# Kernel optimization log

Hardware: AMD Instinct MI355X
Metric: run time of the kernel (lower is better)

The kernel has to match this reference:

```python
import jax, jax.numpy as jnp
import numpy as np

N = 2048
D_T = 256; D_F = 256
E_T = 32; E_F = 32; E_C = 128
C = 5; Q = 512


def setup_inputs() -> dict:
    key = jax.random.key(0)
    ks = jax.random.split(key, 12)
    # full graph minus self-loops, row-major (matches dense_to_sparse ordering)
    r, c = np.meshgrid(np.arange(N), np.arange(N), indexing='ij')
    m = r != c
    edge_index = jnp.asarray(np.stack([r[m], c[m]]), dtype=jnp.int32)  # [2, N*(N-1)]
    E = edge_index.shape[1]
    s = 0.02
    return {
        'time_features': jax.random.normal(ks[0], (N, D_T), jnp.float32),
        'edge_index': edge_index,
        'time_edge_weight': jax.random.uniform(ks[1], (E,), jnp.float32),
        'freq_features': jax.random.normal(ks[2], (N, D_F), jnp.float32),
        'freq_edge_weight': jax.random.uniform(ks[3], (E,), jnp.float32),
        'labels': jax.random.randint(ks[4], (N,), 0, C, jnp.int32),
        'num_classes': C,
        'query_size': Q,
        'Wt': jax.random.normal(ks[5], (D_T, E_T), jnp.float32) * s,
        'bt': jnp.zeros((E_T,), jnp.float32),
        'Wf': jax.random.normal(ks[6], (D_F, E_F), jnp.float32) * s,
        'bf': jnp.zeros((E_F,), jnp.float32),
        'Wc': jax.random.normal(ks[7], (E_T + E_F + C, E_C), jnp.float32) * s,
        'bc': jnp.zeros((E_C,), jnp.float32),
        'Wo': jax.random.normal(ks[8], (E_C, C), jnp.float32) * s,
        'bo': jnp.zeros((C,), jnp.float32),
    }


def _gcn(x, A, W, b):
    # torch_geometric GCNConv: D^{-1/2}(A + I)D^{-1/2} (X W) + b
    n = A.shape[0]
    Ah = A + jnp.eye(n, dtype=A.dtype)
    deg = Ah.sum(axis=1)
    dis = jnp.where(deg > 0, jax.lax.rsqrt(deg), 0.0)
    return (dis[:, None] * Ah * dis[None, :]) @ (x @ W) + b


def reference(time_features, edge_index, time_edge_weight, freq_features,
              freq_edge_weight, labels, num_classes, query_size,
              Wt, bt, Wf, bf, Wc, bc, Wo, bo):
    n = time_features.shape[0]
    lrelu = lambda z: jax.nn.leaky_relu(z, 0.01)

    def dense_adj(w):  # A[dst, src] = w
        return jnp.zeros((n, n), w.dtype).at[edge_index[1], edge_index[0]].add(w)

    te = lrelu(_gcn(time_features, dense_adj(time_edge_weight), Wt, bt))
    fe = lrelu(_gcn(freq_features, dense_adj(freq_edge_weight), Wf, bf))

    # to_one_hot: one_hot[:n - query_size, labels] = 1 -> support rows get 1 in
    # every column that appears anywhere in `labels`
    cols = jnp.zeros((num_classes,), te.dtype).at[labels].set(1.0)
    rowmask = (jnp.arange(n) < (n - query_size)).astype(te.dtype)
    one_hot = rowmask[:, None] * cols[None, :]

    feats = jnp.concatenate([te, fe, one_hot], axis=-1)  # [n, E_T+E_F+C]

    # graph_construction (no_grad in original): 1 / (L1 distance over the
    # non-one-hot dims + 1e-5), zero diagonal
    fd = jax.lax.stop_gradient(feats[:, : feats.shape[1] - num_classes])
    dist = jnp.sum(jnp.abs(fd[:, None, :] - fd[None, :, :]), axis=-1)  # [n, n]
    Aw = (1.0 / (dist + 1e-5)) * (1.0 - jnp.eye(n, dtype=feats.dtype))

    emb = lrelu(_gcn(feats, Aw, Wc, bc))
    return emb @ Wo + bo
```

## Files before the change

### kernel.cpp

```cpp
#include <hip/hip_runtime.h>
#include <hip/hip_bf16.h>

#define N 2048
#define NM1 2047
#define DT 256
#define ET 32
#define EC 128
#define NC 5
#define FS 80
#define FD 69
#define KC_ET 16
#define KC_EC 16

typedef __hip_bfloat16 bf16;

__global__ __launch_bounds__(256) void k_deg_label_xw(const float* __restrict__ tw,
                                                      const float* __restrict__ fw,
                                                      const int* __restrict__ labels,
                                                      const float* __restrict__ Xt,
                                                      const float* __restrict__ Wt,
                                                      const float* __restrict__ Xf,
                                                      const float* __restrict__ Wf,
                                                      float* __restrict__ degT,
                                                      float* __restrict__ degF,
                                                      float* __restrict__ cols,
                                                      float* __restrict__ Yt,
                                                      float* __restrict__ Yf){
    int b = blockIdx.x;
    int t = threadIdx.x;
    if (b < 512){
        int p = (b & 7)*256 + t;
        if (p >= NM1) return;
        int s0 = (b >> 3)*32;
        float lowT=0.f, highT=0.f, lowF=0.f, highF=0.f;
        #pragma unroll 8
        for (int r = 0; r < 32; ++r){
            int s = s0 + r;
            float vt = tw[(size_t)s*NM1 + p];
            float vf = fw[(size_t)s*NM1 + p];
            if (s <= p){ highT += vt; highF += vf; }
            else       { lowT  += vt; lowF  += vf; }
        }
        atomicAdd(&degT[p],   lowT);
        atomicAdd(&degF[p],   lowF);
        atomicAdd(&degT[p+1], highT);
        atomicAdd(&degF[p+1], highF);
        return;
    }
    if (b == 512){
        __shared__ float lc[NC];
        if (t < NC) lc[t] = 0.f;
        __syncthreads();
        for (int i = t; i < N; i += 256){
            int l = labels[i];
            if (l >= 0 && l < NC) lc[l] = 1.f;
        }
        __syncthreads();
        if (t < NC) cols[t] = lc[t];
        return;
    }
    int idx = b - 513;
    const float* X = (idx & 256) ? Xf : Xt;
    const float* W = (idx & 256) ? Wf : Wt;
    float*       Y = (idx & 256) ? Yf : Yt;
    __shared__ float Ws[DT*ET];
    __shared__ float Xs[8*DT];
    for (int j = t; j < DT*ET; j += 256) Ws[j] = W[j];
    int i0 = (idx & 255)*8;
    for (int j = t; j < 8*DT; j += 256) Xs[j] = X[(size_t)i0*DT + j];
    __syncthreads();
    int r = t >> 5, f = t & 31;
    const float* xr = Xs + r*DT;
    float acc = 0.f;
    #pragma unroll 8
    for (int d = 0; d < DT; ++d) acc += xr[d]*Ws[d*ET+f];
    Y[(size_t)(i0+r)*ET+f] = acc;
}

__global__ __launch_bounds__(256) void k_agg_et(const float* __restrict__ tw,
                                                const float* __restrict__ fw,
                                                const float* __restrict__ Yt,
                                                const float* __restrict__ Yf,
                                                const float* __restrict__ degT,
                                                const float* __restrict__ degF,
                                                float* __restrict__ Pt,
                                                float* __restrict__ Pf){
    __shared__ float Ast[64*68];
    __shared__ float Asf[64*68];
    __shared__ float Zst[64*ET];
    __shared__ float Zsf[64*ET];
    int t = threadIdx.x;
    int i0 = blockIdx.x*64;
    int kc = blockIdx.y;
    int k0 = kc*128;
    int g  = t >> 7;
    int tt = t & 127;
    int ig = tt >> 3, fg = tt & 7;
    int r0 = ig*4, c0 = fg*4;
    const float* As = g ? Asf : Ast;
    const float* Zs = g ? Zsf : Zst;
    float acc[4][4];
    #pragma unroll
    for (int u=0;u<4;++u)
        #pragma unroll
        for (int v=0;v<4;++v) acc[u][v]=0.f;

    for (int kt = 0; kt < 2; ++kt){
        int kb = k0 + kt*64;
        #pragma unroll
        for (int e = 0; e < 16; ++e){
            int id = t + e*256;
            int k_l = id >> 6, i_l = id & 63;
            int k = kb + k_l;
            int gi = i0 + i_l;
            float vt, vf;
            if (gi == k){ vt = 0.f; vf = 0.f; }
            else {
                size_t base = (size_t)k*NM1 + gi - (gi > k ? 1 : 0);
                vt = tw[base]; vf = fw[base];
            }
            Ast[k_l*68 + i_l] = vt;
            Asf[k_l*68 + i_l] = vf;
        }
        #pragma unroll
        for (int e = 0; e < 2; ++e){
            int id = t + e*256;
            int row = id >> 3;
            int c4  = (id & 7)*4;
            float rdT = rsqrtf(1.f + degT[kb+row]);
            float rdF = rsqrtf(1.f + degF[kb+row]);
            float4 yt = *(const float4*)&Yt[(size_t)(kb+row)*ET + c4];
            float4 yf = *(const float4*)&Yf[(size_t)(kb+row)*ET + c4];
            yt.x*=rdT; yt.y*=rdT; yt.z*=rdT; yt.w*=rdT;
            yf.x*=rdF; yf.y*=rdF; yf.z*=rdF; yf.w*=rdF;
            *(float4*)&Zst[row*ET + c4] = yt;
            *(float4*)&Zsf[row*ET + c4] = yf;
        }
        __syncthreads();
        for (int k = 0; k < 64; ++k){
            float4 a = *(const float4*)&As[k*68 + r0];
            float4 z = *(const float4*)&Zs[k*ET + c0];
            const float* ap = (const float*)&a;
            const float* zp = (const float*)&z;
            #pragma unroll
            for (int u = 0; u < 4; ++u)
                #pragma unroll
                for (int v = 0; v < 4; ++v)
                    acc[u][v] += ap[u]*zp[v];
        }
        __syncthreads();
    }
    float* P = g ? Pf : Pt;
    #pragma unroll
    for (int u = 0; u < 4; ++u){
        size_t ii = (size_t)(i0 + r0 + u);
        float4 o;
        float* po = (float*)&o;
        #pragma unroll
        for (int v = 0; v < 4; ++v) po[v]=acc[u][v];
        *(float4*)&P[(size_t)kc*(N*ET) + ii*ET + c0] = o;
    }
}

__global__ __launch_bounds__(256) void k_feats_epi(const float* __restrict__ Pt,
                                                   const float* __restrict__ Pf,
                                                   const float* __restrict__ Yt,
                                                   const float* __restrict__ Yf,
                                                   const float* __restrict__ degT,
                                                   const float* __restrict__ degF,
                                                   const float* __restrict__ bt,
                                                   const float* __restrict__ bfv,
                                                   const float* __restrict__ cols,
                                                   const int* __restrict__ qsize,
                                                   float* __restrict__ feats){
    int idx = blockIdx.x*256 + threadIdx.x;
    int i = idx >> 6;
    int f = idx & 63;
    float s, rd, b;
    if (f < ET){
        rd = rsqrtf(1.f + degT[i]);
        s = rd*Yt[(size_t)i*ET + f];
        #pragma unroll
        for (int kc = 0; kc < KC_ET; ++kc) s += Pt[(size_t)kc*(N*ET) + (size_t)i*ET + f];
        b = bt[f];
    } else {
        int g = f - ET;
        rd = rsqrtf(1.f + degF[i]);
        s = rd*Yf[(size_t)i*ET + g];
        #pragma unroll
        for (int kc = 0; kc < KC_ET; ++kc) s += Pf[(size_t)kc*(N*ET) + (size_t)i*ET + g];
        b = bfv[g];
    }
    float v = rd*s + b;
    feats[(size_t)i*FS + f] = v > 0.f ? v : 0.01f*v;
    if (f < NC){
        int nsup = N - qsize[0];
        feats[(size_t)i*FS + 2*ET + f] = (i < nsup) ? cols[f] : 0.f;
    }
}

__global__ __launch_bounds__(256) void k_build_aw(const float* __restrict__ feats,
                                                  float* __restrict__ Aw,
                                                  float* __restrict__ dsum){
    __shared__ float fiT[64*68];
    __shared__ float fjT[64*68];
    int t = threadIdx.x;
    int i0 = blockIdx.x*64, j0 = blockIdx.y*64;
    {
        int row = t >> 2;
        int cb  = (t & 3)*16;
        const float4* si = (const float4*)(feats + (size_t)(i0+row)*FS + cb);
        const float4* sj = (const float4*)(feats + (size_t)(j0+row)*FS + cb);
        #pragma unroll
        for (int s = 0; s < 4; ++s){
            float4 v = si[s];
            float4 w = sj[s];
            int c = cb + s*4;
            fiT[(c+0)*68+row]=v.x; fiT[(c+1)*68+row]=v.y; fiT[(c+2)*68+row]=v.z; fiT[(c+3)*68+row]=v.w;
            fjT[(c+0)*68+row]=w.x; fjT[(c+1)*68+row]=w.y; fjT[(c+2)*68+row]=w.z; fjT[(c+3)*68+row]=w.w;
        }
    }
    __syncthreads();
    int tx = t & 15, ty = t >> 4;
    float acc[4][4];
    #pragma unroll
    for (int u=0;u<4;++u)
        #pragma unroll
        for (int v=0;v<4;++v) acc[u][v]=0.f;
    for (int d = 0; d < 64; ++d){
        float4 a4 = *(const float4*)&fiT[d*68 + ty*4];
        float4 b4 = *(const float4*)&fjT[d*68 + tx*4];
        const float* ap = (const float*)&a4;
        const float* bp = (const float*)&b4;
        #pragma unroll
        for (int u = 0; u < 4; ++u)
            #pragma unroll
            for (int v = 0; v < 4; ++v)
                acc[u][v] += fabsf(ap[u]-bp[v]);
    }
    #pragma unroll
    for (int u = 0; u < 4; ++u){
        int gi = i0 + ty*4 + u;
        float4 o;
        float* po = (float*)&o;
        #pragma unroll
        for (int v = 0; v < 4; ++v){
            int gj = j0 + tx*4 + v;
            po[v] = (gi==gj) ? 1.0f : 1.0f/(acc[u][v] + 1e-5f);
        }
        *(float4*)&Aw[(size_t)gi*N + j0 + tx*4] = o;
        float rs = (po[0]+po[1]) + (po[2]+po[3]);
        rs += __shfl_xor(rs, 1);
        rs += __shfl_xor(rs, 2);
        rs += __shfl_xor(rs, 4);
        rs += __shfl_xor(rs, 8);
        if (tx == 0) atomicAdd(&dsum[gi], rs);
    }
}

__global__ __launch_bounds__(256) void k_featswc(const float* __restrict__ feats,
                                                 const float* __restrict__ Wc,
                                                 const float* __restrict__ dsum,
                                                 float* __restrict__ Zc){
    __shared__ float Wcs[FD*EC];
    __shared__ float fr[8][FD+3];
    int t = threadIdx.x;
    for (int idx = t; idx < FD*EC; idx += 256) Wcs[idx] = Wc[idx];
    int i0 = blockIdx.x*8;
    for (int idx = t; idx < 8*FD; idx += 256){
        int r = idx / FD;
        int c = idx - r*FD;
        fr[r][c] = feats[(size_t)(i0+r)*FS + c];
    }
    __syncthreads();
    int f  = t & 127;
    int rh = t >> 7;
    for (int rr = 0; rr < 4; ++rr){
        int r = rh*4 + rr;
        float acc = 0.f;
        #pragma unroll
        for (int d = 0; d < FD; ++d) acc += fr[r][d]*Wcs[d*EC+f];
        int i = i0 + r;
        Zc[(size_t)i*EC + f] = rsqrtf(dsum[i])*acc;
    }
}

__global__ __launch_bounds__(256) void k_agg_ec(const float* __restrict__ Aw,
                                                const float* __restrict__ Zc,
                                                float* __restrict__ Pe){
    __shared__ float As[128*128];
    __shared__ float Zs[128*128];
    int t = threadIdx.x;
    int i0 = blockIdx.x*128;
    int kc = blockIdx.y;
    int k0 = kc*128;
    int rg = t >> 4;
    int cg = t & 15;
    int r0 = rg*8;
    int ca = cg*4, cb = 64 + cg*4;

    #pragma unroll
    for (int e = 0; e < 16; ++e){
        int id = t + e*256;
        int k_l = id >> 5;
        int i4  = (id & 31)*4;
        *(float4*)&As[k_l*128 + i4] = *(const float4*)&Aw[(size_t)(k0+k_l)*N + i0 + i4];
    }
    #pragma unroll
    for (int e = 0; e < 16; ++e){
        int id = t + e*256;
        int k_l = id >> 5;
        int c4  = (id & 31)*4;
        *(float4*)&Zs[k_l*128 + c4] = *(const float4*)&Zc[(size_t)(k0+k_l)*EC + c4];
    }
    __syncthreads();

    float acc[8][8];
    #pragma unroll
    for (int u=0;u<8;++u)
        #pragma unroll
        for (int v=0;v<8;++v) acc[u][v]=0.f;

    for (int k = 0; k < 128; ++k){
        float4 a0 = *(const float4*)&As[k*128 + r0];
        float4 a1 = *(const float4*)&As[k*128 + r0 + 4];
        float4 z0 = *(const float4*)&Zs[k*128 + ca];
        float4 z1 = *(const float4*)&Zs[k*128 + cb];
        float a8[8] = {a0.x,a0.y,a0.z,a0.w,a1.x,a1.y,a1.z,a1.w};
        float zl[4] = {z0.x,z0.y,z0.z,z0.w};
        float zh[4] = {z1.x,z1.y,z1.z,z1.w};
        #pragma unroll
        for (int u = 0; u < 8; ++u){
            #pragma unroll
            for (int v = 0; v < 4; ++v){
                acc[u][v]   += a8[u]*zl[v];
                acc[u][v+4] += a8[u]*zh[v];
            }
        }
    }
    #pragma unroll
    for (int u = 0; u < 8; ++u){
        size_t ii = (size_t)(i0 + r0 + u);
        float4 o0, o1;
        float* p0 = (float*)&o0; float* p1 = (float*)&o1;
        #pragma unroll
        for (int v = 0; v < 4; ++v){ p0[v]=acc[u][v]; p1[v]=acc[u][v+4]; }
        *(float4*)&Pe[(size_t)kc*(N*EC) + ii*EC + ca] = o0;
        *(float4*)&Pe[(size_t)kc*(N*EC) + ii*EC + cb] = o1;
    }
}

__global__ __launch_bounds__(256) void k_embfinal(const float* __restrict__ Pe,
                                                  const float* __restrict__ dsum,
                                                  const float* __restrict__ bc,
                                                  const float* __restrict__ Wo,
                                                  const float* __restrict__ bo,
                                                  float* __restrict__ out){
    __shared__ float vs[2][EC];
    __shared__ float Wos[EC*NC];
    __shared__ float bos[NC];
    int t = threadIdx.x;
    for (int idx = t; idx < EC*NC; idx += 256) Wos[idx] = Wo[idx];
    if (t < NC) bos[t] = bo[t];
    int rr = t >> 7, f = t & 127;
    int i = blockIdx.x*2 + rr;
    size_t idx = (size_t)i*EC + f;
    float s = 0.f;
    #pragma unroll
    for (int kc = 0; kc < KC_EC; ++kc) s += Pe[(size_t)kc*(N*EC) + idx];
    float v = rsqrtf(dsum[i])*s + bc[f];
    vs[rr][f] = v > 0.f ? v : 0.01f*v;
    __syncthreads();
    if (t < 2*NC){
        int r = t / NC;
        int c = t - r*NC;
        float a = bos[c];
        #pragma unroll 8
        for (int f2 = 0; f2 < EC; ++f2) a += vs[r][f2]*Wos[f2*NC+c];
        out[(size_t)(blockIdx.x*2 + r)*NC + c] = a;
    }
}

extern "C" void kernel_launch(void* const* d_in, const int* in_sizes, int n_in,
                              void* d_out, int out_size, void* d_ws, size_t ws_size,
                              hipStream_t stream) {
    const float* time_features = (const float*)d_in[0];
    const float* tw            = (const float*)d_in[2];
    const float* freq_features = (const float*)d_in[3];
    const float* fw            = (const float*)d_in[4];
    const int*   labels        = (const int*)d_in[5];
    const int*   qsize         = (const int*)d_in[7];
    const float* Wt  = (const float*)d_in[8];
    const float* bt  = (const float*)d_in[9];
    const float* Wf  = (const float*)d_in[10];
    const float* bfv = (const float*)d_in[11];
    const float* Wc  = (const float*)d_in[12];
    const float* bc  = (const float*)d_in[13];
    const float* Wo  = (const float*)d_in[14];
    const float* bo  = (const float*)d_in[15];
    float* out = (float*)d_out;

    float* ws    = (float*)d_ws;
    float* Yt    = ws;
    float* Yf    = Yt + (size_t)N*ET;
    float* Zc    = Yf + (size_t)N*ET;
    float* degT  = Zc + (size_t)N*EC;
    float* degF  = degT + N;
    float* dsum  = degF + N;
    float* colsb = dsum + N;
    float* feats = colsb + 8;
    float* Aw    = feats + (size_t)N*FS;
    float* Pt    = Aw + (size_t)N*N;
    float* Pf    = Pt + (size_t)KC_ET*N*ET;
    float* Pe    = Pf + (size_t)KC_ET*N*ET;

    hipMemsetAsync(degT, 0, 3*N*sizeof(float), stream);
    k_deg_label_xw<<<1025, 256, 0, stream>>>(tw, fw, labels,
                                             time_features, Wt, freq_features, Wf,
                                             degT, degF, colsb, Yt, Yf);
    k_agg_et<<<dim3(N/64, KC_ET), 256, 0, stream>>>(tw, fw, Yt, Yf, degT, degF, Pt, Pf);
    k_feats_epi<<<(N*64)/256, 256, 0, stream>>>(Pt, Pf, Yt, Yf, degT, degF,
                                                bt, bfv, colsb, qsize, feats);
    k_build_aw<<<dim3(N/64, N/64), 256, 0, stream>>>(feats, Aw, dsum);
    k_featswc<<<N/8, 256, 0, stream>>>(feats, Wc, dsum, Zc);
    k_agg_ec<<<dim3(N/128, KC_EC), 256, 0, stream>>>(Aw, Zc, Pe);
    k_embfinal<<<N/2, 256, 0, stream>>>(Pe, dsum, bc, Wo, bo, out);
}
```

Measured before the change: 209.1 us.

## Fuse all stages into one persistent kernel with software grid barriers

```diff
diff --git a/kernel.cpp b/kernel.cpp
--- a/kernel.cpp
+++ b/kernel.cpp
@@ -11,373 +11,372 @@
 #define FD 69
 #define KC_ET 16
 #define KC_EC 16
+#define NB 256
 
 typedef __hip_bfloat16 bf16;
 
-__global__ __launch_bounds__(256) void k_deg_label_xw(const float* __restrict__ tw,
-                                                      const float* __restrict__ fw,
-                                                      const int* __restrict__ labels,
-                                                      const float* __restrict__ Xt,
-                                                      const float* __restrict__ Wt,
-                                                      const float* __restrict__ Xf,
-                                                      const float* __restrict__ Wf,
-                                                      float* __restrict__ degT,
-                                                      float* __restrict__ degF,
-                                                      float* __restrict__ cols,
-                                                      float* __restrict__ Yt,
-                                                      float* __restrict__ Yf){
+__device__ __forceinline__ void gridbar(int* cnt, int target){
+    __syncthreads();
+    if (threadIdx.x == 0){
+        __threadfence();
+        atomicAdd(cnt, 1);
+        while (atomicAdd(cnt, 0) < target) __builtin_amdgcn_s_sleep(1);
+        __threadfence();
+    }
+    __syncthreads();
+}
+
+__global__ __launch_bounds__(256, 1)
+void k_mega(const float* __restrict__ tw, const float* __restrict__ fw,
+            const int* __restrict__ labels,
+            const float* __restrict__ Xt, const float* __restrict__ Wt,
+            const float* __restrict__ Xf, const float* __restrict__ Wf,
+            const float* __restrict__ bt, const float* __restrict__ bfv,
+            const int* __restrict__ qsize,
+            const float* __restrict__ Wc, const float* __restrict__ bc,
+            const float* __restrict__ Wo, const float* __restrict__ bo,
+            float* degT, float* degF, float* dsum, int* cnt, float* colsb,
+            float* Yt, float* Yf, float* Zc, float* feats, float* Aw,
+            float* Pt, float* Pf, float* Pe, float* out){
+    __shared__ float lds[32768];
     int b = blockIdx.x;
     int t = threadIdx.x;
-    if (b < 512){
-        int p = (b & 7)*256 + t;
-        if (p >= NM1) return;
-        int s0 = (b >> 3)*32;
-        float lowT=0.f, highT=0.f, lowF=0.f, highF=0.f;
-        #pragma unroll 8
-        for (int r = 0; r < 32; ++r){
-            int s = s0 + r;
-            float vt = tw[(size_t)s*NM1 + p];
-            float vf = fw[(size_t)s*NM1 + p];
-            if (s <= p){ highT += vt; highF += vf; }
-            else       { lowT  += vt; lowF  += vf; }
-        }
-        atomicAdd(&degT[p],   lowT);
-        atomicAdd(&degF[p],   lowF);
-        atomicAdd(&degT[p+1], highT);
-        atomicAdd(&degF[p+1], highF);
-        return;
-    }
-    if (b == 512){
-        __shared__ float lc[NC];
-        if (t < NC) lc[t] = 0.f;
+
+    for (int v = b; v < 1025; v += NB){
+        if (v < 512){
+            int p = (v & 7)*256 + t;
+            if (p < NM1){
+                int s0 = (v >> 3)*32;
+                float lowT=0.f, highT=0.f, lowF=0.f, highF=0.f;
+                #pragma unroll 8
+                for (int r = 0; r < 32; ++r){
+                    int s = s0 + r;
+                    float vt = tw[(size_t)s*NM1 + p];
+                    float vf = fw[(size_t)s*NM1 + p];
+                    if (s <= p){ highT += vt; highF += vf; }
+                    else       { lowT  += vt; lowF  += vf; }
+                }
+                atomicAdd(&degT[p],   lowT);
+                atomicAdd(&degF[p],   lowF);
+                atomicAdd(&degT[p+1], highT);
+                atomicAdd(&degF[p+1], highF);
+            }
+        } else if (v == 512){
+            float* lc = lds;
+            if (t < NC) lc[t] = 0.f;
+            __syncthreads();
+            for (int i = t; i < N; i += 256){
+                int l = labels[i];
+                if (l >= 0 && l < NC) lc[l] = 1.f;
+            }
+            __syncthreads();
+            if (t < NC) colsb[t] = lc[t];
+            __syncthreads();
+        } else {
+            int idx = v - 513;
+            const float* X = (idx & 256) ? Xf : Xt;
+            const float* W = (idx & 256) ? Wf : Wt;
+            float*       Y = (idx & 256) ? Yf : Yt;
+            float* Ws = lds;
+            float* Xs = lds + 8192;
+            for (int j = t; j < DT*ET; j += 256) Ws[j] = W[j];
+            int i0 = (idx & 255)*8;
+            for (int j = t; j < 8*DT; j += 256) Xs[j] = X[(size_t)i0*DT + j];
+            __syncthreads();
+            int r = t >> 5, f = t & 31;
+            const float* xr = Xs + r*DT;
+            float acc = 0.f;
+            #pragma unroll 8
+            for (int d = 0; d < DT; ++d) acc += xr[d]*Ws[d*ET+f];
+            Y[(size_t)(i0+r)*ET+f] = acc;
+            __syncthreads();
+        }
+    }
+    gridbar(cnt, 1*NB);
+
+    {
+        float* Ast = lds;
+        float* Asf = lds + 64*68;
+        float* Zst = lds + 2*64*68;
+        float* Zsf = lds + 2*64*68 + 64*32;
+        int g  = t >> 7;
+        int tt = t & 127;
+        int ig = tt >> 3, fg = tt & 7;
+        int r0 = ig*4, c0 = fg*4;
+        const float* As = g ? Asf : Ast;
+        const float* Zs = g ? Zsf : Zst;
+        for (int vv = 0; vv < 2; ++vv){
+            int v = b*2 + vv;
+            int i0 = (v & 31)*64;
+            int kc = v >> 5;
+            int k0 = kc*128;
+            float acc[4][4];
+            #pragma unroll
+            for (int u=0;u<4;++u)
+                #pragma unroll
+                for (int w=0;w<4;++w) acc[u][w]=0.f;
+            for (int kt = 0; kt < 2; ++kt){
+                int kb = k0 + kt*64;
+                #pragma unroll
+                for (int e = 0; e < 16; ++e){
+                    int id = t + e*256;
+                    int k_l = id >> 6, i_l = id & 63;
+                    int k = kb + k_l;
+                    int gi = i0 + i_l;
+                    float vt, vf;
+                    if (gi == k){ vt = 0.f; vf = 0.f; }
+                    else {
+                        size_t base = (size_t)k*NM1 + gi - (gi > k ? 1 : 0);
+                        vt = tw[base]; vf = fw[base];
+                    }
+                    Ast[k_l*68 + i_l] = vt;
+                    Asf[k_l*68 + i_l] = vf;
+                }
+                #pragma unroll
+                for (int e = 0; e < 2; ++e){
+                    int id = t + e*256;
+                    int row = id >> 3;
+                    int c4  = (id & 7)*4;
+                    float rdT = rsqrtf(1.f + degT[kb+row]);
+                    float rdF = rsqrtf(1.f + degF[kb+row]);
+                    float4 yt = *(const float4*)&Yt[(size_t)(kb+row)*ET + c4];
+                    float4 yf = *(const float4*)&Yf[(size_t)(kb+row)*ET + c4];
+                    yt.x*=rdT; yt.y*=rdT; yt.z*=rdT; yt.w*=rdT;
+                    yf.x*=rdF; yf.y*=rdF; yf.z*=rdF; yf.w*=rdF;
+                    *(float4*)&Zst[row*ET + c4] = yt;
+                    *(float4*)&Zsf[row*ET + c4] = yf;
+                }
+                __syncthreads();
+                for (int k = 0; k < 64; ++k){
+                    float4 a = *(const float4*)&As[k*68 + r0];
+                    float4 z = *(const float4*)&Zs[k*ET + c0];
+                    const float* ap = (const float*)&a;
+                    const float* zp = (const float*)&z;
+                    #pragma unroll
+                    for (int u = 0; u < 4; ++u)
+                        #pragma unroll
+                        for (int w = 0; w < 4; ++w)
+                            acc[u][w] += ap[u]*zp[w];
+                }
+                __syncthreads();
+            }
+            float* P = g ? Pf : Pt;
+            #pragma unroll
+            for (int u = 0; u < 4; ++u){
+                size_t ii = (size_t)(i0 + r0 + u);
+                float4 o;
+                float* po = (float*)&o;
+                #pragma unroll
+                for (int w = 0; w < 4; ++w) po[w]=acc[u][w];
+                *(float4*)&P[(size_t)kc*(N*ET) + ii*ET + c0] = o;
+            }
+        }
+    }
+    gridbar(cnt, 2*NB);
+
+    for (int vv = 0; vv < 2; ++vv){
+        int idx = (b*2+vv)*256 + t;
+        int i = idx >> 6;
+        int f = idx & 63;
+        float s, rd, bb;
+        if (f < ET){
+            rd = rsqrtf(1.f + degT[i]);
+            s = rd*Yt[(size_t)i*ET + f];
+            #pragma unroll
+            for (int kc = 0; kc < KC_ET; ++kc) s += Pt[(size_t)kc*(N*ET) + (size_t)i*ET + f];
+            bb = bt[f];
+        } else {
+            int g2 = f - ET;
+            rd = rsqrtf(1.f + degF[i]);
+            s = rd*Yf[(size_t)i*ET + g2];
+            #pragma unroll
+            for (int kc = 0; kc < KC_ET; ++kc) s += Pf[(size_t)kc*(N*ET) + (size_t)i*ET + g2];
+            bb = bfv[g2];
+        }
+        float vx = rd*s + bb;
+        feats[(size_t)i*FS + f] = vx > 0.f ? vx : 0.01f*vx;
+        if (f < NC){
+            int nsup = N - qsize[0];
+            feats[(size_t)i*FS + 2*ET + f] = (i < nsup) ? colsb[f] : 0.f;
+        }
+    }
+    gridbar(cnt, 3*NB);
+
+    {
+        float* fiT = lds;
+        float* fjT = lds + 64*68;
+        int tx = t & 15, ty = t >> 4;
+        for (int vv = 0; vv < 4; ++vv){
+            int v = b*4 + vv;
+            int i0 = (v & 31)*64, j0 = (v >> 5)*64;
+            {
+                int row = t >> 2;
+                int cb  = (t & 3)*16;
+                const float4* si = (const float4*)(feats + (size_t)(i0+row)*FS + cb);
+                const float4* sj = (const float4*)(feats + (size_t)(j0+row)*FS + cb);
+                #pragma unroll
+                for (int s = 0; s < 4; ++s){
+                    float4 vx = si[s];
+                    float4 w = sj[s];
+                    int c = cb + s*4;
+                    fiT[(c+0)*68+row]=vx.x; fiT[(c+1)*68+row]=vx.y; fiT[(c+2)*68+row]=vx.z; fiT[(c+3)*68+row]=vx.w;
+                    fjT[(c+0)*68+row]=w.x;  fjT[(c+1)*68+row]=w.y;  fjT[(c+2)*68+row]=w.z;  fjT[(c+3)*68+row]=w.w;
+                }
+            }
+            __syncthreads();
+            float acc[4][4];
+            #pragma unroll
+            for (int u=0;u<4;++u)
+                #pragma unroll
+                for (int w=0;w<4;++w) acc[u][w]=0.f;
+            for (int d = 0; d < 64; ++d){
+                float4 a4 = *(const float4*)&fiT[d*68 + ty*4];
+                float4 b4 = *(const float4*)&fjT[d*68 + tx*4];
+                const float* ap = (const float*)&a4;
+                const float* bp = (const float*)&b4;
+                #pragma unroll
+                for (int u = 0; u < 4; ++u)
+                    #pragma unroll
+                    for (int w = 0; w < 4; ++w)
+                        acc[u][w] += fabsf(ap[u]-bp[w]);
+            }
+            #pragma unroll
+            for (int u = 0; u < 4; ++u){
+                int gi = i0 + ty*4 + u;
+                float4 o;
+                float* po = (float*)&o;
+                #pragma unroll
+                for (int w = 0; w < 4; ++w){
+                    int gj = j0 + tx*4 + w;
+                    po[w] = (gi==gj) ? 1.0f : 1.0f/(acc[u][w] + 1e-5f);
+                }
+                *(float4*)&Aw[(size_t)gi*N + j0 + tx*4] = o;
+                float rs = (po[0]+po[1]) + (po[2]+po[3]);
+                rs += __shfl_xor(rs, 1);
+                rs += __shfl_xor(rs, 2);
+                rs += __shfl_xor(rs, 4);
+                rs += __shfl_xor(rs, 8);
+                if (tx == 0) atomicAdd(&dsum[gi], rs);
+            }
+            __syncthreads();
+        }
+    }
+    gridbar(cnt, 4*NB);
+
+    {
+        float* Wcs = lds;
+        float* fr  = lds + 8832;
+        for (int idx = t; idx < FD*EC; idx += 256) Wcs[idx] = Wc[idx];
+        int i0 = b*8;
+        for (int idx = t; idx < 8*FD; idx += 256){
+            int r = idx / FD;
+            int c = idx - r*FD;
+            fr[r*(FD+3) + c] = feats[(size_t)(i0+r)*FS + c];
+        }
         __syncthreads();
-        for (int i = t; i < N; i += 256){
-            int l = labels[i];
-            if (l >= 0 && l < NC) lc[l] = 1.f;
+        int f  = t & 127;
+        int rh = t >> 7;
+        for (int rr = 0; rr < 4; ++rr){
+            int r = rh*4 + rr;
+            float acc = 0.f;
+            #pragma unroll
+            for (int d = 0; d < FD; ++d) acc += fr[r*(FD+3)+d]*Wcs[d*EC+f];
+            int i = i0 + r;
+            Zc[(size_t)i*EC + f] = rsqrtf(dsum[i])*acc;
         }
         __syncthreads();
-        if (t < NC) cols[t] = lc[t];
-        return;
-    }
-    int idx = b - 513;
-    const float* X = (idx & 256) ? Xf : Xt;
-    const float* W = (idx & 256) ? Wf : Wt;
-    float*       Y = (idx & 256) ? Yf : Yt;
-    __shared__ float Ws[DT*ET];
-    __shared__ float Xs[8*DT];
-    for (int j = t; j < DT*ET; j += 256) Ws[j] = W[j];
-    int i0 = (idx & 255)*8;
-    for (int j = t; j < 8*DT; j += 256) Xs[j] = X[(size_t)i0*DT + j];
-    __syncthreads();
-    int r = t >> 5, f = t & 31;
-    const float* xr = Xs + r*DT;
-    float acc = 0.f;
-    #pragma unroll 8
-    for (int d = 0; d < DT; ++d) acc += xr[d]*Ws[d*ET+f];
-    Y[(size_t)(i0+r)*ET+f] = acc;
-}
-
-__global__ __launch_bounds__(256) void k_agg_et(const float* __restrict__ tw,
-                                                const float* __restrict__ fw,
-                                                const float* __restrict__ Yt,
-                                                const float* __restrict__ Yf,
-                                                const float* __restrict__ degT,
-                                                const float* __restrict__ degF,
-                                                float* __restrict__ Pt,
-                                                float* __restrict__ Pf){
-    __shared__ float Ast[64*68];
-    __shared__ float Asf[64*68];
-    __shared__ float Zst[64*ET];
-    __shared__ float Zsf[64*ET];
-    int t = threadIdx.x;
-    int i0 = blockIdx.x*64;
-    int kc = blockIdx.y;
-    int k0 = kc*128;
-    int g  = t >> 7;
-    int tt = t & 127;
-    int ig = tt >> 3, fg = tt & 7;
-    int r0 = ig*4, c0 = fg*4;
-    const float* As = g ? Asf : Ast;
-    const float* Zs = g ? Zsf : Zst;
-    float acc[4][4];
-    #pragma unroll
-    for (int u=0;u<4;++u)
-        #pragma unroll
-        for (int v=0;v<4;++v) acc[u][v]=0.f;
-
-    for (int kt = 0; kt < 2; ++kt){
-        int kb = k0 + kt*64;
+    }
+    gridbar(cnt, 5*NB);
+
+    {
+        float* As = lds;
+        float* Zs = lds + 16384;
+        int i0 = (b & 15)*128;
+        int kc = b >> 4;
+        int k0 = kc*128;
+        int rg = t >> 4;
+        int cg = t & 15;
+        int r0 = rg*8;
+        int ca = cg*4, cb2 = 64 + cg*4;
         #pragma unroll
         for (int e = 0; e < 16; ++e){
             int id = t + e*256;
-            int k_l = id >> 6, i_l = id & 63;
-            int k = kb + k_l;
-            int gi = i0 + i_l;
-            float vt, vf;
-            if (gi == k){ vt = 0.f; vf = 0.f; }
-            else {
-                size_t base = (size_t)k*NM1 + gi - (gi > k ? 1 : 0);
-                vt = tw[base]; vf = fw[base];
-            }
-            Ast[k_l*68 + i_l] = vt;
-            Asf[k_l*68 + i_l] = vf;
+            int k_l = id >> 5;
+            int i4  = (id & 31)*4;
+            *(float4*)&As[k_l*128 + i4] = *(const float4*)&Aw[(size_t)(k0+k_l)*N + i0 + i4];
         }
         #pragma unroll
-        for (int e = 0; e < 2; ++e){
+        for (int e = 0; e < 16; ++e){
             int id = t + e*256;
-            int row = id >> 3;
-            int c4  = (id & 7)*4;
-            float rdT = rsqrtf(1.f + degT[kb+row]);
-            float rdF = rsqrtf(1.f + degF[kb+row]);
-            float4 yt = *(const float4*)&Yt[(size_t)(kb+row)*ET + c4];
-            float4 yf = *(const float4*)&Yf[(size_t)(kb+row)*ET + c4];
-            yt.x*=rdT; yt.y*=rdT; yt.z*=rdT; yt.w*=rdT;
-            yf.x*=rdF; yf.y*=rdF; yf.z*=rdF; yf.w*=rdF;
-            *(float4*)&Zst[row*ET + c4] = yt;
-            *(float4*)&Zsf[row*ET + c4] = yf;
+            int k_l = id >> 5;
+            int c4  = (id & 31)*4;
+            *(float4*)&Zs[k_l*128 + c4] = *(const float4*)&Zc[(size_t)(k0+k_l)*EC + c4];
         }
         __syncthreads();
-        for (int k = 0; k < 64; ++k){
-            float4 a = *(const float4*)&As[k*68 + r0];
-            float4 z = *(const float4*)&Zs[k*ET + c0];
-            const float* ap = (const float*)&a;
-            const float* zp = (const float*)&z;
-            #pragma unroll
-            for (int u = 0; u < 4; ++u)
-                #pragma unroll
-                for (int v = 0; v < 4; ++v)
-                    acc[u][v] += ap[u]*zp[v];
-        }
-        __syncthreads();
-    }
-    float* P = g ? Pf : Pt;
-    #pragma unroll
-    for (int u = 0; u < 4; ++u){
-        size_t ii = (size_t)(i0 + r0 + u);
-        float4 o;
-        float* po = (float*)&o;
+        float acc[8][8];
         #pragma unroll
-        for (int v = 0; v < 4; ++v) po[v]=acc[u][v];
-        *(float4*)&P[(size_t)kc*(N*ET) + ii*ET + c0] = o;
-    }
-}
-
-__global__ __launch_bounds__(256) void k_feats_epi(const float* __restrict__ Pt,
-                                                   const float* __restrict__ Pf,
-                                                   const float* __restrict__ Yt,
-                                                   const float* __restrict__ Yf,
-                                                   const float* __restrict__ degT,
-                                                   const float* __restrict__ degF,
-                                                   const float* __restrict__ bt,
-                                                   const float* __restrict__ bfv,
-                                                   const float* __restrict__ cols,
-                                                   const int* __restrict__ qsize,
-                                                   float* __restrict__ feats){
-    int idx = blockIdx.x*256 + threadIdx.x;
-    int i = idx >> 6;
-    int f = idx & 63;
-    float s, rd, b;
-    if (f < ET){
-        rd = rsqrtf(1.f + degT[i]);
-        s = rd*Yt[(size_t)i*ET + f];
-        #pragma unroll
-        for (int kc = 0; kc < KC_ET; ++kc) s += Pt[(size_t)kc*(N*ET) + (size_t)i*ET + f];
-        b = bt[f];
-    } else {
-        int g = f - ET;
-        rd = rsqrtf(1.f + degF[i]);
-        s = rd*Yf[(size_t)i*ET + g];
-        #pragma unroll
-        for (int kc = 0; kc < KC_ET; ++kc) s += Pf[(size_t)kc*(N*ET) + (size_t)i*ET + g];
-        b = bfv[g];
-    }
-    float v = rd*s + b;
-    feats[(size_t)i*FS + f] = v > 0.f ? v : 0.01f*v;
-    if (f < NC){
-        int nsup = N - qsize[0];
-        feats[(size_t)i*FS + 2*ET + f] = (i < nsup) ? cols[f] : 0.f;
-    }
-}
-
-__global__ __launch_bounds__(256) void k_build_aw(const float* __restrict__ feats,
-                                                  float* __restrict__ Aw,
-                                                  float* __restrict__ dsum){
-    __shared__ float fiT[64*68];
-    __shared__ float fjT[64*68];
-    int t = threadIdx.x;
-    int i0 = blockIdx.x*64, j0 = blockIdx.y*64;
-    {
-        int row = t >> 2;
-        int cb  = (t & 3)*16;
-        const float4* si = (const float4*)(feats + (size_t)(i0+row)*FS + cb);
-        const float4* sj = (const float4*)(feats + (size_t)(j0+row)*FS + cb);
-        #pragma unroll
-        for (int s = 0; s < 4; ++s){
-            float4 v = si[s];
-            float4 w = sj[s];
-            int c = cb + s*4;
-            fiT[(c+0)*68+row]=v.x; fiT[(c+1)*68+row]=v.y; fiT[(c+2)*68+row]=v.z; fiT[(c+3)*68+row]=v.w;
-            fjT[(c+0)*68+row]=w.x; fjT[(c+1)*68+row]=w.y; fjT[(c+2)*68+row]=w.z; fjT[(c+3)*68+row]=w.w;
-        }
-    }
-    __syncthreads();
-    int tx = t & 15, ty = t >> 4;
-    float acc[4][4];
-    #pragma unroll
-    for (int u=0;u<4;++u)
-        #pragma unroll
-        for (int v=0;v<4;++v) acc[u][v]=0.f;
-    for (int d = 0; d < 64; ++d){
-        float4 a4 = *(const float4*)&fiT[d*68 + ty*4];
-        float4 b4 = *(const float4*)&fjT[d*68 + tx*4];
-        const float* ap = (const float*)&a4;
-        const float* bp = (const float*)&b4;
-        #pragma unroll
-        for (int u = 0; u < 4; ++u)
-            #pragma unroll
-            for (int v = 0; v < 4; ++v)
-                acc[u][v] += fabsf(ap[u]-bp[v]);
-    }
-    #pragma unroll
-    for (int u = 0; u < 4; ++u){
-        int gi = i0 + ty*4 + u;
-        float4 o;
-        float* po = (float*)&o;
-        #pragma unroll
-        for (int v = 0; v < 4; ++v){
-            int gj = j0 + tx*4 + v;
-            po[v] = (gi==gj) ? 1.0f : 1.0f/(acc[u][v] + 1e-5f);
-        }
-        *(float4*)&Aw[(size_t)gi*N + j0 + tx*4] = o;
-        float rs = (po[0]+po[1]) + (po[2]+po[3]);
-        rs += __shfl_xor(rs, 1);
-        rs += __shfl_xor(rs, 2);
-        rs += __shfl_xor(rs, 4);
-        rs += __shfl_xor(rs, 8);
-        if (tx == 0) atomicAdd(&dsum[gi], rs);
-    }
-}
-
-__global__ __launch_bounds__(256) void k_featswc(const float* __restrict__ feats,
-                                                 const float* __restrict__ Wc,
-                                                 const float* __restrict__ dsum,
-                                                 float* __restrict__ Zc){
-    __shared__ float Wcs[FD*EC];
-    __shared__ float fr[8][FD+3];
-    int t = threadIdx.x;
-    for (int idx = t; idx < FD*EC; idx += 256) Wcs[idx] = Wc[idx];
-    int i0 = blockIdx.x*8;
-    for (int idx = t; idx < 8*FD; idx += 256){
-        int r = idx / FD;
-        int c = idx - r*FD;
-        fr[r][c] = feats[(size_t)(i0+r)*FS + c];
-    }
-    __syncthreads();
-    int f  = t & 127;
-    int rh = t >> 7;
-    for (int rr = 0; rr < 4; ++rr){
-        int r = rh*4 + rr;
-        float acc = 0.f;
-        #pragma unroll
-        for (int d = 0; d < FD; ++d) acc += fr[r][d]*Wcs[d*EC+f];
-        int i = i0 + r;
-        Zc[(size_t)i*EC + f] = rsqrtf(dsum[i])*acc;
-    }
-}
-
-__global__ __launch_bounds__(256) void k_agg_ec(const float* __restrict__ Aw,
-                                                const float* __restrict__ Zc,
-                                                float* __restrict__ Pe){
-    __shared__ float As[128*128];
-    __shared__ float Zs[128*128];
-    int t = threadIdx.x;
-    int i0 = blockIdx.x*128;
-    int kc = blockIdx.y;
-    int k0 = kc*128;
-    int rg = t >> 4;
-    int cg = t & 15;
-    int r0 = rg*8;
-    int ca = cg*4, cb = 64 + cg*4;
-
-    #pragma unroll
-    for (int e = 0; e < 16; ++e){
-        int id = t + e*256;
-        int k_l = id >> 5;
-        int i4  = (id & 31)*4;
-        *(float4*)&As[k_l*128 + i4] = *(const float4*)&Aw[(size_t)(k0+k_l)*N + i0 + i4];
-    }
-    #pragma unroll
-    for (int e = 0; e < 16; ++e){
-        int id = t + e*256;
-        int k_l = id >> 5;
-        int c4  = (id & 31)*4;
-        *(float4*)&Zs[k_l*128 + c4] = *(const float4*)&Zc[(size_t)(k0+k_l)*EC + c4];
-    }
-    __syncthreads();
-
-    float acc[8][8];
-    #pragma unroll
-    for (int u=0;u<8;++u)
-        #pragma unroll
-        for (int v=0;v<8;++v) acc[u][v]=0.f;
-
-    for (int k = 0; k < 128; ++k){
-        float4 a0 = *(const float4*)&As[k*128 + r0];
-        float4 a1 = *(const float4*)&As[k*128 + r0 + 4];
-        float4 z0 = *(const float4*)&Zs[k*128 + ca];
-        float4 z1 = *(const float4*)&Zs[k*128 + cb];
-        float a8[8] = {a0.x,a0.y,a0.z,a0.w,a1.x,a1.y,a1.z,a1.w};
-        float zl[4] = {z0.x,z0.y,z0.z,z0.w};
-        float zh[4] = {z1.x,z1.y,z1.z,z1.w};
+        for (int u=0;u<8;++u)
+            #pragma unroll
+            for (int w=0;w<8;++w) acc[u][w]=0.f;
+        for (int k = 0; k < 128; ++k){
+            float4 a0 = *(const float4*)&As[k*128 + r0];
+            float4 a1 = *(const float4*)&As[k*128 + r0 + 4];
+            float4 z0 = *(const float4*)&Zs[k*128 + ca];
+            float4 z1 = *(const float4*)&Zs[k*128 + cb2];
+            float a8[8] = {a0.x,a0.y,a0.z,a0.w,a1.x,a1.y,a1.z,a1.w};
+            float zl[4] = {z0.x,z0.y,z0.z,z0.w};
+            float zh[4] = {z1.x,z1.y,z1.z,z1.w};
+            #pragma unroll
+            for (int u = 0; u < 8; ++u){
+                #pragma unroll
+                for (int w = 0; w < 4; ++w){
+                    acc[u][w]   += a8[u]*zl[w];
+                    acc[u][w+4] += a8[u]*zh[w];
+                }
+            }
+        }
         #pragma unroll
         for (int u = 0; u < 8; ++u){
-            #pragma unroll
-            for (int v = 0; v < 4; ++v){
-                acc[u][v]   += a8[u]*zl[v];
-                acc[u][v+4] += a8[u]*zh[v];
-            }
-        }
-    }
-    #pragma unroll
-    for (int u = 0; u < 8; ++u){
-        size_t ii = (size_t)(i0 + r0 + u);
-        float4 o0, o1;
-        float* p0 = (float*)&o0; float* p1 = (float*)&o1;
-        #pragma unroll
-        for (int v = 0; v < 4; ++v){ p0[v]=acc[u][v]; p1[v]=acc[u][v+4]; }
-        *(float4*)&Pe[(size_t)kc*(N*EC) + ii*EC + ca] = o0;
-        *(float4*)&Pe[(size_t)kc*(N*EC) + ii*EC + cb] = o1;
-    }
-}
-
-__global__ __launch_bounds__(256) void k_embfinal(const float* __restrict__ Pe,
-                                                  const float* __restrict__ dsum,
-                                                  const float* __restrict__ bc,
-                                                  const float* __restrict__ Wo,
-                                                  const float* __restrict__ bo,
-                                                  float* __restrict__ out){
-    __shared__ float vs[2][EC];
-    __shared__ float Wos[EC*NC];
-    __shared__ float bos[NC];
-    int t = threadIdx.x;
-    for (int idx = t; idx < EC*NC; idx += 256) Wos[idx] = Wo[idx];
-    if (t < NC) bos[t] = bo[t];
-    int rr = t >> 7, f = t & 127;
-    int i = blockIdx.x*2 + rr;
-    size_t idx = (size_t)i*EC + f;
-    float s = 0.f;
-    #pragma unroll
-    for (int kc = 0; kc < KC_EC; ++kc) s += Pe[(size_t)kc*(N*EC) + idx];
-    float v = rsqrtf(dsum[i])*s + bc[f];
-    vs[rr][f] = v > 0.f ? v : 0.01f*v;
-    __syncthreads();
-    if (t < 2*NC){
-        int r = t / NC;
-        int c = t - r*NC;
-        float a = bos[c];
-        #pragma unroll 8
-        for (int f2 = 0; f2 < EC; ++f2) a += vs[r][f2]*Wos[f2*NC+c];
-        out[(size_t)(blockIdx.x*2 + r)*NC + c] = a;
+            size_t ii = (size_t)(i0 + r0 + u);
+            float4 o0, o1;
+            float* p0 = (float*)&o0; float* p1 = (float*)&o1;
+            #pragma unroll
+            for (int w = 0; w < 4; ++w){ p0[w]=acc[u][w]; p1[w]=acc[u][w+4]; }
+            *(float4*)&Pe[(size_t)kc*(N*EC) + ii*EC + ca]  = o0;
+            *(float4*)&Pe[(size_t)kc*(N*EC) + ii*EC + cb2] = o1;
+        }
+        __syncthreads();
+    }
+    gridbar(cnt, 6*NB);
+
+    {
+        float* Wos = lds;
+        float* bos = lds + 640;
+        float* vs  = lds + 656;
+        for (int idx = t; idx < EC*NC; idx += 256) Wos[idx] = Wo[idx];
+        if (t < NC) bos[t] = bo[t];
+        __syncthreads();
+        int rr = t >> 7, f = t & 127;
+        for (int vv = 0; vv < 4; ++vv){
+            int v = b*4 + vv;
+            int i = v*2 + rr;
+            size_t idx = (size_t)i*EC + f;
+            float s = 0.f;
+            #pragma unroll
+            for (int kc = 0; kc < KC_EC; ++kc) s += Pe[(size_t)kc*(N*EC) + idx];
+            float vx = rsqrtf(dsum[i])*s + bc[f];
+            vs[rr*EC + f] = vx > 0.f ? vx : 0.01f*vx;
+            __syncthreads();
+            if (t < 2*NC){
+                int r = t / NC;
+                int c = t - r*NC;
+                float a = bos[c];
+                #pragma unroll 8
+                for (int f2 = 0; f2 < EC; ++f2) a += vs[r*EC+f2]*Wos[f2*NC+c];
+                out[(size_t)(v*2 + r)*NC + c] = a;
+            }
+            __syncthreads();
+        }
     }
 }
 
@@ -401,28 +400,24 @@
     float* out = (float*)d_out;
 
     float* ws    = (float*)d_ws;
-    float* Yt    = ws;
+    float* degT  = ws;
+    float* degF  = degT + N;
+    float* dsum  = degF + N;
+    int*   cnt   = (int*)(dsum + N);
+    float* colsb = dsum + N + 4;
+    float* Yt    = colsb + 12;
     float* Yf    = Yt + (size_t)N*ET;
     float* Zc    = Yf + (size_t)N*ET;
-    float* degT  = Zc + (size_t)N*EC;
-    float* degF  = degT + N;
-    float* dsum  = degF + N;
-    float* colsb = dsum + N;
-    float* feats = colsb + 8;
+    float* feats = Zc + (size_t)N*EC;
     float* Aw    = feats + (size_t)N*FS;
     float* Pt    = Aw + (size_t)N*N;
     float* Pf    = Pt + (size_t)KC_ET*N*ET;
     float* Pe    = Pf + (size_t)KC_ET*N*ET;
 
-    hipMemsetAsync(degT, 0, 3*N*sizeof(float), stream);
-    k_deg_label_xw<<<1025, 256, 0, stream>>>(tw, fw, labels,
-                                             time_features, Wt, freq_features, Wf,
-                                             degT, degF, colsb, Yt, Yf);
-    k_agg_et<<<dim3(N/64, KC_ET), 256, 0, stream>>>(tw, fw, Yt, Yf, degT, degF, Pt, Pf);
-    k_feats_epi<<<(N*64)/256, 256, 0, stream>>>(Pt, Pf, Yt, Yf, degT, degF,
-                                                bt, bfv, colsb, qsize, feats);
-    k_build_aw<<<dim3(N/64, N/64), 256, 0, stream>>>(feats, Aw, dsum);
-    k_featswc<<<N/8, 256, 0, stream>>>(feats, Wc, dsum, Zc);
-    k_agg_ec<<<dim3(N/128, KC_EC), 256, 0, stream>>>(Aw, Zc, Pe);
-    k_embfinal<<<N/2, 256, 0, stream>>>(Pe, dsum, bc, Wo, bo, out);
+    hipMemsetAsync(degT, 0, (3*N+4)*sizeof(float), stream);
+    k_mega<<<NB, 256, 0, stream>>>(tw, fw, labels,
+                                   time_features, Wt, freq_features, Wf,
+                                   bt, bfv, qsize, Wc, bc, Wo, bo,
+                                   degT, degF, dsum, cnt, colsb,
+                                   Yt, Yf, Zc, feats, Aw, Pt, Pf, Pe, out);
 }
```

New measurement: 356.1 us. 1.7x slower.
